# Optimization experiments

Hardware: AMD Instinct MI355X
Metric: run time of the kernel (lower is better)

Reference implementation:

```python
import jax, jax.numpy as jnp
import numpy as np

N = 21  # nodes per graph (20 laser sectors + 1 robot node)
MAX_RANGE = 10.0
_bound = np.linspace(-np.pi / 2 - 0.03, np.pi / 2, 21, dtype=np.float32)[:-1]
_angles = _bound + np.float32(np.pi / 20)
ANGLE_FEAT = jnp.asarray(np.stack([np.sin(_angles), np.cos(_angles)], 1), dtype=jnp.float32)  # [20,2]


def _build_nodes(state24):
    # state24: [B,24] -> node features [B,21,7]
    B = state24.shape[0]
    laser = state24[:, :20, None] / MAX_RANGE                       # [B,20,1]
    angle = jnp.broadcast_to(ANGLE_FEAT[None], (B, 20, 2))          # [B,20,2]
    sector = jnp.concatenate([laser, angle, jnp.zeros((B, 20, 4), state24.dtype)], -1)  # [B,20,7]
    robot = jnp.concatenate([jnp.zeros((B, 1, 3), state24.dtype), state24[:, None, 20:]], -1)  # [B,1,7]
    return jnp.concatenate([sector, robot], axis=1)                 # [B,21,7]


def _gatv2(x, Wl, Wr, att, bias, heads, dim):
    # GATv2 over a fully-connected graph with self-loops (dense all-pairs).
    # e_ij = att . leaky_relu(Wl x_j + Wr x_i); alpha = softmax_j; out_i = sum_j alpha_ij (Wl x_j)
    B = x.shape[0]
    gl = (x @ Wl).reshape(B, N, heads, dim)  # source transform [B,j,H,D]
    gr = (x @ Wr).reshape(B, N, heads, dim)  # target transform [B,i,H,D]
    s = jax.nn.leaky_relu(gl[:, None] + gr[:, :, None], negative_slope=0.2)  # [B,i,j,H,D]
    e = jnp.einsum('bijhd,hd->bijh', s, att)                                  # [B,i,j,H]
    alpha = jax.nn.softmax(e, axis=2)                                          # softmax over sources j
    out = jnp.einsum('bijh,bjhd->bihd', alpha, gl).reshape(B, N, heads * dim)
    return out + bias


def setup_inputs() -> dict:
    key = jax.random.key(0)
    ks = jax.random.split(key, 16)
    r = lambda k, shape, s: (jax.random.normal(k, shape, dtype=jnp.float32) * s)
    B = 1024
    return {
        'state24': jax.random.normal(ks[0], (B, 24), dtype=jnp.float32),
        'Wl1': r(ks[1], (7, 256), 0.3), 'Wr1': r(ks[2], (7, 256), 0.3),
        'att1': r(ks[3], (4, 64), 0.1), 'b1': r(ks[4], (256,), 0.02),
        'Wl2': r(ks[5], (256, 64), 0.06), 'Wr2': r(ks[6], (256, 64), 0.06),
        'att2': r(ks[7], (1, 64), 0.1), 'b2': r(ks[8], (64,), 0.02),
        'fc1_w': r(ks[9], (64, 256), 0.12), 'fc1_b': r(ks[10], (256,), 0.02),
        'fc2_w': r(ks[11], (256, 256), 0.06), 'fc2_b': r(ks[12], (256,), 0.02),
        'fc3_w': r(ks[13], (256, 2), 0.06), 'fc3_b': r(ks[14], (2,), 0.02),
    }


def reference(state24, Wl1, Wr1, att1, b1, Wl2, Wr2, att2, b2,
              fc1_w, fc1_b, fc2_w, fc2_b, fc3_w, fc3_b):
    x = _build_nodes(state24)                               # [B,21,7]
    h = jax.nn.elu(_gatv2(x, Wl1, Wr1, att1, b1, 4, 64))    # [B,21,256]
    h = _gatv2(h, Wl2, Wr2, att2, b2, 1, 64)                # [B,21,64]
    nfv = jnp.mean(h, axis=1)                               # global_mean_pool -> [B,64]
    h = jax.nn.relu(nfv @ fc1_w + fc1_b)
    h = jax.nn.relu(h @ fc2_w + fc2_b)
    return jnp.tanh(h @ fc3_w + fc3_b)                      # [B,2]
```

## Files before the change

kernel.cpp:

```cpp
#include <hip/hip_runtime.h>
#include <hip/hip_fp16.h>
#include <math.h>

#define PI_D 3.141592653589793

typedef _Float16 h2 __attribute__((ext_vector_type(2)));
typedef _Float16 h4 __attribute__((ext_vector_type(4)));
typedef _Float16 h8 __attribute__((ext_vector_type(8)));
typedef unsigned short us8 __attribute__((ext_vector_type(8)));
typedef __fp16 f16v2 __attribute__((ext_vector_type(2)));
typedef __fp16 f16v8 __attribute__((ext_vector_type(8)));
typedef float f32x4 __attribute__((ext_vector_type(4)));

#define STR1 264
#define STR2H 72

#define SV(v, a, b) __builtin_shufflevector(v, v, a, b)

static __device__ __forceinline__ h2 pack_h2(float a, float b) {
    return __builtin_bit_cast(h2, __builtin_amdgcn_cvt_pkrtz(a, b));
}

static __device__ __forceinline__ float fdot2(h2 a, h2 b, float c) {
    return __builtin_amdgcn_fdot2(__builtin_bit_cast(f16v2, a),
                                  __builtin_bit_cast(f16v2, b), c, false);
}

static __device__ __forceinline__ h8 habs8(h8 x) {
    us8 u = __builtin_bit_cast(us8, x);
    us8 m = {0x7fff, 0x7fff, 0x7fff, 0x7fff, 0x7fff, 0x7fff, 0x7fff, 0x7fff};
    return __builtin_bit_cast(h8, (us8)(u & m));
}

static __device__ __forceinline__ f32x4 mfma16(h8 a, h8 b, f32x4 c) {
    return __builtin_amdgcn_mfma_f32_16x16x32_f16(
        __builtin_bit_cast(f16v8, a), __builtin_bit_cast(f16v8, b), c, 0, 0, 0);
}

static __device__ __forceinline__ void wave_fence() {
    asm volatile("" ::: "memory");
#if __has_builtin(__builtin_amdgcn_wave_barrier)
    __builtin_amdgcn_wave_barrier();
#endif
    asm volatile("" ::: "memory");
}

__global__ __launch_bounds__(256) void pack_weights_kernel(
    const float* __restrict__ Wl2, const float* __restrict__ Wr2,
    const float* __restrict__ fc1_w, const float* __restrict__ fc2_w,
    h8* __restrict__ ws)
{
    int idx = blockIdx.x * 256 + threadIdx.x;
    if (idx < 4096) {
        const float* W = idx < 2048 ? Wl2 : Wr2;
        int t = idx & 2047;
        int ntile = t >> 9, rem = t & 511;
        int kchunk = rem >> 6, lane = rem & 63;
        int n = ntile * 16 + (lane & 15);
        int k0 = kchunk * 32 + (lane >> 4) * 8;
        h8 o;
        #pragma unroll
        for (int j = 0; j < 8; ++j) o[j] = (_Float16)W[(k0 + j) * 64 + n];
        ws[idx] = o;
    } else if (idx < 6144) {
        int t = idx - 4096;
        int k2 = t >> 6, c = t & 63;
        h8 o;
        #pragma unroll
        for (int q = 0; q < 4; ++q) {
            o[2 * q]     = (_Float16)fc1_w[(2 * k2) * 256 + 4 * c + q];
            o[2 * q + 1] = (_Float16)fc1_w[(2 * k2 + 1) * 256 + 4 * c + q];
        }
        ws[idx] = o;
    } else {
        int t = idx - 6144;
        int k2 = t >> 6, c = t & 63;
        h8 o;
        #pragma unroll
        for (int q = 0; q < 4; ++q) {
            o[2 * q]     = (_Float16)fc2_w[(2 * k2) * 256 + 4 * c + q];
            o[2 * q + 1] = (_Float16)fc2_w[(2 * k2 + 1) * 256 + 4 * c + q];
        }
        ws[idx] = o;
    }
}

__global__ __launch_bounds__(256, 2) void actor_fused_kernel(
    const float* __restrict__ state24,
    const float* __restrict__ Wl1, const float* __restrict__ Wr1,
    const float* __restrict__ att1, const float* __restrict__ b1,
    const float* __restrict__ att2, const float* __restrict__ b2,
    const float* __restrict__ fc1_b, const float* __restrict__ fc2_b,
    const float* __restrict__ fc3_w, const float* __restrict__ fc3_b,
    const h8* __restrict__ wsL, const h8* __restrict__ wsR,
    const h8* __restrict__ wsF1, const h8* __restrict__ wsF2,
    float* __restrict__ out, int B)
{
    const int bix = blockIdx.x;
    const int tid = threadIdx.x;
    const int smp0 = 2 * bix;
    if (smp0 >= B) return;
    const int smp1 = (smp0 + 1 < B) ? smp0 + 1 : smp0;

    __shared__ float sinL[20], cosL[20], laserL[2][20], robotL[2][4];
    __shared__ __align__(16) h2 attLh[128];
    __shared__ __align__(16) h2 att2Lh[32];
    __shared__ __align__(16) _Float16 gr1h[2][22 * STR1];
    __shared__ __align__(16) union {
        struct { _Float16 gl1h[2][22 * STR1];
                 float ePf[2][128 * 24];
                 float uv[2][168]; } p1;
        struct { _Float16 gl2h[2][21 * STR2H];
                 _Float16 gr2h[2][21 * STR2H];
                 _Float16 gl2hT[2][64 * 32];
                 float e2[2][32 * 24];
                 float u2v2[2][42];
                 float red[2][4][256];
                 _Float16 nfvh[2][64]; _Float16 hah[2][256]; _Float16 hbh[2][256]; } p2;
    } U;

    if (tid < 20) {
        double step = (PI_D + 0.03) / 20.0;
        float bound = (float)(-PI_D / 2.0 - 0.03 + (double)tid * step);
        float ang = bound + (float)(PI_D / 20.0);
        sinL[tid] = sinf(ang);
        cosL[tid] = cosf(ang);
        laserL[0][tid] = state24[smp0 * 24 + tid] * 0.1f;
        laserL[1][tid] = state24[smp1 * 24 + tid] * 0.1f;
    }
    if (tid >= 32 && tid < 40) {
        int s = (tid - 32) >> 2, q = (tid - 32) & 3;
        robotL[s][q] = state24[(s ? smp1 : smp0) * 24 + 20 + q];
    }
    if (tid < 128) {
        float2 ap = ((const float2*)att1)[tid];
        attLh[tid] = pack_h2(0.4f * ap.x, 0.4f * ap.y);
    }
    if (tid >= 128 && tid < 160) {
        float2 ap = ((const float2*)att2)[tid - 128];
        att2Lh[tid - 128] = pack_h2(0.4f * ap.x, 0.4f * ap.y);
    }
    __syncthreads();

    {
        const int h = tid >> 6;
        const int lane = tid & 63;

        {
            const int cp = lane & 31;
            const int half = lane >> 5;
            const int d2 = h * 32 + cp;
            float2 wl[7], wr[7];
            #pragma unroll
            for (int k = 0; k < 7; k++) {
                wl[k] = ((const float2*)Wl1)[k * 128 + d2];
                wr[k] = ((const float2*)Wr1)[k * 128 + d2];
            }
            if (half == 0) {
                h2 zz2 = {};
                #pragma unroll
                for (int s = 0; s < 2; ++s) {
                    ((h2*)(U.p1.gl1h[s] + 21 * STR1))[d2] = zz2;
                    ((h2*)(gr1h[s] + 21 * STR1))[d2] = zz2;
                }
            }
            const int base = half * 11;
            #pragma unroll
            for (int nn = 0; nn < 11; ++nn) {
                int node = base + nn;
                if (node < 21) {
                    #pragma unroll
                    for (int s = 0; s < 2; ++s) {
                        float a0, a1, b0, b1v;
                        if (node < 20) {
                            float l = laserL[s][node], sv = sinL[node], c = cosL[node];
                            a0 = l * wl[0].x + sv * wl[1].x + c * wl[2].x;
                            a1 = l * wl[0].y + sv * wl[1].y + c * wl[2].y;
                            b0 = l * wr[0].x + sv * wr[1].x + c * wr[2].x;
                            b1v = l * wr[0].y + sv * wr[1].y + c * wr[2].y;
                        } else {
                            float r0 = robotL[s][0], r1 = robotL[s][1], r2 = robotL[s][2], r3 = robotL[s][3];
                            a0 = r0 * wl[3].x + r1 * wl[4].x + r2 * wl[5].x + r3 * wl[6].x;
                            a1 = r0 * wl[3].y + r1 * wl[4].y + r2 * wl[5].y + r3 * wl[6].y;
                            b0 = r0 * wr[3].x + r1 * wr[4].x + r2 * wr[5].x + r3 * wr[6].x;
                            b1v = r0 * wr[3].y + r1 * wr[4].y + r2 * wr[5].y + r3 * wr[6].y;
                        }
                        ((h2*)(U.p1.gl1h[s] + node * STR1))[d2] = pack_h2(a0, a1);
                        ((h2*)(gr1h[s] + node * STR1))[d2] = pack_h2(b0, b1v);
                    }
                }
            }
        }
        wave_fence();

        {
            h2 ar[32];
            #pragma unroll
            for (int q = 0; q < 32; ++q) ar[q] = attLh[h * 32 + q];

            #pragma unroll
            for (int s = 0; s < 2; ++s) {
                for (int it = 0; it < 7; ++it) {
                    int q = it * 64 + lane;
                    if (q < 441) {
                        int i = q / 21;
                        int j = q - i * 21;
                        const h8* gA8 = (const h8*)(U.p1.gl1h[s] + j * STR1 + h * 64);
                        const h8* gB8 = (const h8*)(gr1h[s] + i * STR1 + h * 64);
                        float m0 = 0.f, m1 = 0.f;
                        #pragma unroll
                        for (int ch = 0; ch < 8; ++ch) {
                            h8 x = gA8[ch] + gB8[ch];
                            h8 ax = habs8(x);
                            m0 = fdot2(SV(ax, 0, 1), ar[ch * 4 + 0], m0);
                            m1 = fdot2(SV(ax, 2, 3), ar[ch * 4 + 1], m1);
                            m0 = fdot2(SV(ax, 4, 5), ar[ch * 4 + 2], m0);
                            m1 = fdot2(SV(ax, 6, 7), ar[ch * 4 + 3], m1);
                        }
                        U.p1.ePf[s][(h * 32 + i) * 24 + j] = m0 + m1;
                    }
                }
            }
            if (lane < 42) {
                int isV = lane >= 21;
                int idx = isV ? lane - 21 : lane;
                #pragma unroll
                for (int s = 0; s < 2; ++s) {
                    const _Float16* rowp = (isV ? (const _Float16*)gr1h[s]
                                                : (const _Float16*)U.p1.gl1h[s]) + idx * STR1 + h * 64;
                    const h8* row8 = (const h8*)rowp;
                    float l0 = 0.f, l1 = 0.f;
                    #pragma unroll
                    for (int ch = 0; ch < 8; ++ch) {
                        h8 g = row8[ch];
                        l0 = fdot2(SV(g, 0, 1), ar[ch * 4 + 0], l0);
                        l1 = fdot2(SV(g, 2, 3), ar[ch * 4 + 1], l1);
                        l0 = fdot2(SV(g, 4, 5), ar[ch * 4 + 2], l0);
                        l1 = fdot2(SV(g, 6, 7), ar[ch * 4 + 3], l1);
                    }
                    U.p1.uv[s][(isV ? 84 : 0) + h * 21 + idx] = l0 + l1;
                }
            }
        }
        wave_fence();

        if (lane < 42) {
            int s = lane >= 21;
            int i = lane - s * 21;
            int r = h * 32 + i;
            float* row = U.p1.ePf[s] + r * 24;
            const float* uu = U.p1.uv[s] + h * 21;
            float vi = 1.5f * U.p1.uv[s][84 + h * 21 + i];
            float ebuf[21];
            float m = -1e30f;
            #pragma unroll
            for (int j = 0; j < 21; j++) {
                float e = row[j] + 1.5f * uu[j] + vi;
                ebuf[j] = e;
                m = fmaxf(m, e);
            }
            float sum = 0.f;
            #pragma unroll
            for (int j = 0; j < 21; j++) { float v = __expf(ebuf[j] - m); ebuf[j] = v; sum += v; }
            float rinv = 1.f / sum;
            h8* hp8 = (h8*)(U.p1.ePf[s]) + r * 6;
            h8 o0, o1, o2;
            #pragma unroll
            for (int q = 0; q < 8; ++q) o0[q] = (_Float16)(ebuf[q] * rinv);
            #pragma unroll
            for (int q = 0; q < 8; ++q) o1[q] = (_Float16)(ebuf[8 + q] * rinv);
            #pragma unroll
            for (int q = 0; q < 5; ++q) o2[q] = (_Float16)(ebuf[16 + q] * rinv);
            o2[5] = (_Float16)0.f; o2[6] = (_Float16)0.f; o2[7] = (_Float16)0.f;
            h8 zz = {};
            hp8[0] = o0; hp8[1] = o1; hp8[2] = o2;
            hp8[3] = zz; hp8[4] = zz; hp8[5] = zz;
        }
        {
            h8 zz = {};
            for (int z = lane; z < 132; z += 64) {
                int s = z >= 66;
                int zz2 = z - s * 66;
                int rr = zz2 / 6, slot = zz2 - rr * 6;
                ((h8*)U.p1.ePf[s])[(h * 32 + 21 + rr) * 6 + slot] = zz;
            }
        }
        wave_fence();

        {
            const int mcol = lane & 15;
            const int quad = lane >> 4;
            h8 A0s[2], A1s[2];
            #pragma unroll
            for (int s = 0; s < 2; ++s) {
                const h8* Af = (const h8*)U.p1.ePf[s];
                A0s[s] = Af[(h * 32 + mcol) * 6 + quad];
                A1s[s] = Af[(h * 32 + 16 + mcol) * 6 + quad];
            }
            int rowoff[8];
            #pragma unroll
            for (int jj = 0; jj < 8; ++jj) {
                int rr = quad * 8 + jj;
                rowoff[jj] = (rr > 21 ? 21 : rr) * STR1;
            }
            const int colbase = h * 64 + mcol;
            f32x4 z4 = {0.f, 0.f, 0.f, 0.f};
            #pragma unroll
            for (int t = 0; t < 4; ++t) {
                int col = colbase + t * 16;
                float bb = b1[col];
                #pragma unroll
                for (int s = 0; s < 2; ++s) {
                    h8 bv;
                    #pragma unroll
                    for (int jj = 0; jj < 8; ++jj) bv[jj] = U.p1.gl1h[s][rowoff[jj] + col];
                    f32x4 d0 = mfma16(A0s[s], bv, z4);
                    f32x4 d1 = mfma16(A1s[s], bv, z4);
                    #pragma unroll
                    for (int r = 0; r < 4; ++r) {
                        int n0 = quad * 4 + r;
                        float v = d0[r] + bb;
                        v = v > 0.f ? v : __expf(v) - 1.f;
                        gr1h[s][n0 * STR1 + col] = (_Float16)v;
                        int n1 = 16 + quad * 4 + r;
                        if (n1 < 21) {
                            float w2 = d1[r] + bb;
                            w2 = w2 > 0.f ? w2 : __expf(w2) - 1.f;
                            gr1h[s][n1 * STR1 + col] = (_Float16)w2;
                        }
                    }
                }
            }
        }
    }
    __syncthreads();

    {
        const int lane = tid & 63;
        const int w = tid >> 6;
        const int mrow = lane & 15;
        const int quad = lane >> 4;
        int rowA1 = 16 + mrow; if (rowA1 > 21) rowA1 = 21;
        const h8* bL = wsL + w * 512 + lane;
        const h8* bR = wsR + w * 512 + lane;
        f32x4 aL0[2], aL1[2], aR0[2], aR1[2];
        #pragma unroll
        for (int s = 0; s < 2; ++s) {
            aL0[s] = (f32x4){0.f, 0.f, 0.f, 0.f}; aL1[s] = (f32x4){0.f, 0.f, 0.f, 0.f};
            aR0[s] = (f32x4){0.f, 0.f, 0.f, 0.f}; aR1[s] = (f32x4){0.f, 0.f, 0.f, 0.f};
        }
        #pragma unroll
        for (int kc = 0; kc < 8; ++kc) {
            h8 BL = bL[kc * 64];
            h8 BR = bR[kc * 64];
            #pragma unroll
            for (int s = 0; s < 2; ++s) {
                h8 A0 = *(const h8*)(gr1h[s] + mrow * STR1 + quad * 8 + kc * 32);
                h8 A1 = *(const h8*)(gr1h[s] + rowA1 * STR1 + quad * 8 + kc * 32);
                aL0[s] = mfma16(A0, BL, aL0[s]);
                aL1[s] = mfma16(A1, BL, aL1[s]);
                aR0[s] = mfma16(A0, BR, aR0[s]);
                aR1[s] = mfma16(A1, BR, aR1[s]);
            }
        }
        const int col = w * 16 + mrow;
        #pragma unroll
        for (int s = 0; s < 2; ++s) {
            #pragma unroll
            for (int r = 0; r < 4; ++r) {
                int row0 = quad * 4 + r;
                U.p2.gl2h[s][row0 * STR2H + col] = (_Float16)aL0[s][r];
                U.p2.gr2h[s][row0 * STR2H + col] = (_Float16)aR0[s][r];
                int row1 = 16 + row0;
                if (row1 < 21) {
                    U.p2.gl2h[s][row1 * STR2H + col] = (_Float16)aL1[s][r];
                    U.p2.gr2h[s][row1 * STR2H + col] = (_Float16)aR1[s][r];
                }
            }
            h2 lo0 = pack_h2(aL0[s][0], aL0[s][1]);
            h2 hi0 = pack_h2(aL0[s][2], aL0[s][3]);
            h4 p0 = __builtin_shufflevector(lo0, hi0, 0, 1, 2, 3);
            *(h4*)(U.p2.gl2hT[s] + col * 32 + quad * 4) = p0;
            h2 lo1 = pack_h2(aL1[s][0], aL1[s][1]);
            h2 hi1 = pack_h2(aL1[s][2], aL1[s][3]);
            h4 p1 = __builtin_shufflevector(lo1, hi1, 0, 1, 2, 3);
            *(h4*)(U.p2.gl2hT[s] + col * 32 + 16 + quad * 4) = p1;
        }
    }
    __syncthreads();

    {
        h2 ar2[32];
        #pragma unroll
        for (int q = 0; q < 32; ++q) ar2[q] = att2Lh[q];

        #pragma unroll
        for (int it = 0; it < 4; ++it) {
            int t = it * 256 + tid;
            if (t < 882) {
                int s = t >= 441;
                int p = t - s * 441;
                int i = p / 21;
                int j = p - i * 21;
                const h8* gA8 = (const h8*)(U.p2.gl2h[s] + j * STR2H);
                const h8* gB8 = (const h8*)(U.p2.gr2h[s] + i * STR2H);
                float m0 = 0.f, m1 = 0.f;
                #pragma unroll
                for (int ch = 0; ch < 8; ++ch) {
                    h8 x = gA8[ch] + gB8[ch];
                    h8 ax = habs8(x);
                    m0 = fdot2(SV(ax, 0, 1), ar2[ch * 4 + 0], m0);
                    m1 = fdot2(SV(ax, 2, 3), ar2[ch * 4 + 1], m1);
                    m0 = fdot2(SV(ax, 4, 5), ar2[ch * 4 + 2], m0);
                    m1 = fdot2(SV(ax, 6, 7), ar2[ch * 4 + 3], m1);
                }
                U.p2.e2[s][i * 24 + j] = m0 + m1;
            } else if (t < 966) {
                int u = t - 882;
                int s = u >= 42;
                int r = u - s * 42;
                int isV = r >= 21;
                int idx = r - isV * 21;
                const _Float16* rowp = (isV ? U.p2.gr2h[s] : U.p2.gl2h[s]) + idx * STR2H;
                const h8* row8 = (const h8*)rowp;
                float l0 = 0.f, l1 = 0.f;
                #pragma unroll
                for (int ch = 0; ch < 8; ++ch) {
                    h8 g = row8[ch];
                    l0 = fdot2(SV(g, 0, 1), ar2[ch * 4 + 0], l0);
                    l1 = fdot2(SV(g, 2, 3), ar2[ch * 4 + 1], l1);
                    l0 = fdot2(SV(g, 4, 5), ar2[ch * 4 + 2], l0);
                    l1 = fdot2(SV(g, 6, 7), ar2[ch * 4 + 3], l1);
                }
                U.p2.u2v2[s][isV * 21 + idx] = l0 + l1;
            }
        }
    }
    __syncthreads();

    if (tid < 42) {
        int s = tid >= 21;
        int i = tid - s * 21;
        float* row = U.p2.e2[s] + i * 24;
        const float* uu = U.p2.u2v2[s];
        float vi = 1.5f * U.p2.u2v2[s][21 + i];
        float ebuf[21];
        float m = -1e30f;
        #pragma unroll
        for (int j = 0; j < 21; j++) {
            float e = row[j] + 1.5f * uu[j] + vi;
            ebuf[j] = e;
            m = fmaxf(m, e);
        }
        float sum = 0.f;
        #pragma unroll
        for (int j = 0; j < 21; j++) { float v = __expf(ebuf[j] - m); ebuf[j] = v; sum += v; }
        float rinv = 1.f / sum;
        h8* hp8 = (h8*)(U.p2.e2[s]) + i * 6;
        h8 o0, o1, o2;
        #pragma unroll
        for (int q = 0; q < 8; ++q) o0[q] = (_Float16)(ebuf[q] * rinv);
        #pragma unroll
        for (int q = 0; q < 8; ++q) o1[q] = (_Float16)(ebuf[8 + q] * rinv);
        #pragma unroll
        for (int q = 0; q < 5; ++q) o2[q] = (_Float16)(ebuf[16 + q] * rinv);
        o2[5] = (_Float16)0.f; o2[6] = (_Float16)0.f; o2[7] = (_Float16)0.f;
        h8 zz = {};
        hp8[0] = o0; hp8[1] = o1; hp8[2] = o2;
        hp8[3] = zz; hp8[4] = zz; hp8[5] = zz;
    } else if (tid < 174) {
        int z = tid - 42;
        int s = z >= 66;
        int zz2 = z - s * 66;
        int rr = zz2 / 6, slot = zz2 - rr * 6;
        h8 zz = {};
        ((h8*)U.p2.e2[s])[(21 + rr) * 6 + slot] = zz;
    }
    __syncthreads();

    {
        const int lane = tid & 63;
        const int w = tid >> 6;
        const int mcol = lane & 15;
        const int quad = lane >> 4;
        const int col = w * 16 + mcol;
        float bb = b2[col];
        f32x4 z4 = {0.f, 0.f, 0.f, 0.f};
        #pragma unroll
        for (int s = 0; s < 2; ++s) {
            const h8* Af2 = (const h8*)U.p2.e2[s];
            h8 A0 = Af2[mcol * 6 + quad];
            h8 A1 = Af2[(16 + mcol) * 6 + quad];
            h8 bv = *(const h8*)(U.p2.gl2hT[s] + col * 32 + quad * 8);
            f32x4 d0 = mfma16(A0, bv, z4);
            f32x4 d1 = mfma16(A1, bv, z4);
            float sum = (d0[0] + d0[1]) + (d0[2] + d0[3])
                      + (d1[0] + d1[1]) + (d1[2] + d1[3]);
            sum += __shfl_xor(sum, 16, 64);
            sum += __shfl_xor(sum, 32, 64);
            if (quad == 0) U.p2.nfvh[s][col] = (_Float16)(sum * (1.f / 21.f) + bb);
        }
    }
    __syncthreads();

    {
        int c = tid & 63, g = tid >> 6;
        float4 acc0 = {0.f, 0.f, 0.f, 0.f}, acc1 = {0.f, 0.f, 0.f, 0.f};
        #pragma unroll
        for (int kk = 0; kk < 8; ++kk) {
            int k2 = g * 8 + kk;
            h8 w = wsF1[k2 * 64 + c];
            h2 x0 = ((const h2*)U.p2.nfvh[0])[k2];
            h2 x1 = ((const h2*)U.p2.nfvh[1])[k2];
            acc0.x = fdot2(SV(w, 0, 1), x0, acc0.x);
            acc0.y = fdot2(SV(w, 2, 3), x0, acc0.y);
            acc0.z = fdot2(SV(w, 4, 5), x0, acc0.z);
            acc0.w = fdot2(SV(w, 6, 7), x0, acc0.w);
            acc1.x = fdot2(SV(w, 0, 1), x1, acc1.x);
            acc1.y = fdot2(SV(w, 2, 3), x1, acc1.y);
            acc1.z = fdot2(SV(w, 4, 5), x1, acc1.z);
            acc1.w = fdot2(SV(w, 6, 7), x1, acc1.w);
        }
        ((float4*)U.p2.red[0][g])[c] = acc0;
        ((float4*)U.p2.red[1][g])[c] = acc1;
    }
    __syncthreads();
    {
        float bb = fc1_b[tid];
        #pragma unroll
        for (int s = 0; s < 2; ++s) {
            float v = U.p2.red[s][0][tid] + U.p2.red[s][1][tid]
                    + U.p2.red[s][2][tid] + U.p2.red[s][3][tid] + bb;
            U.p2.hah[s][tid] = (_Float16)fmaxf(v, 0.f);
        }
    }
    __syncthreads();

    {
        int c = tid & 63, g = tid >> 6;
        const h8* ha0 = (const h8*)U.p2.hah[0];
        const h8* ha1 = (const h8*)U.p2.hah[1];
        float4 acc0 = {0.f, 0.f, 0.f, 0.f}, acc1 = {0.f, 0.f, 0.f, 0.f};
#define FC2_STEP(q, p)                                                          \
        {                                                                       \
            int k2 = g * 32 + (q) * 4 + (p);                                    \
            h8 w = wsF2[k2 * 64 + c];                                           \
            h2 x0 = __builtin_shufflevector(xa0, xa0, 2 * (p), 2 * (p) + 1);    \
            h2 x1 = __builtin_shufflevector(xa1, xa1, 2 * (p), 2 * (p) + 1);    \
            acc0.x = fdot2(SV(w, 0, 1), x0, acc0.x);                            \
            acc0.y = fdot2(SV(w, 2, 3), x0, acc0.y);                            \
            acc0.z = fdot2(SV(w, 4, 5), x0, acc0.z);                            \
            acc0.w = fdot2(SV(w, 6, 7), x0, acc0.w);                            \
            acc1.x = fdot2(SV(w, 0, 1), x1, acc1.x);                            \
            acc1.y = fdot2(SV(w, 2, 3), x1, acc1.y);                            \
            acc1.z = fdot2(SV(w, 4, 5), x1, acc1.z);                            \
            acc1.w = fdot2(SV(w, 6, 7), x1, acc1.w);                            \
        }
        #pragma unroll
        for (int q = 0; q < 8; ++q) {
            h8 xa0 = ha0[g * 8 + q];
            h8 xa1 = ha1[g * 8 + q];
            FC2_STEP(q, 0)
            FC2_STEP(q, 1)
            FC2_STEP(q, 2)
            FC2_STEP(q, 3)
        }
#undef FC2_STEP
        ((float4*)U.p2.red[0][g])[c] = acc0;
        ((float4*)U.p2.red[1][g])[c] = acc1;
    }
    __syncthreads();
    {
        float bb = fc2_b[tid];
        #pragma unroll
        for (int s = 0; s < 2; ++s) {
            float v = U.p2.red[s][0][tid] + U.p2.red[s][1][tid]
                    + U.p2.red[s][2][tid] + U.p2.red[s][3][tid] + bb;
            U.p2.hbh[s][tid] = (_Float16)fmaxf(v, 0.f);
        }
    }
    __syncthreads();

    {
        int g = tid >> 6;
        int o = g & 1, s = g >> 1;
        int l = tid & 63;
        float sum = 0.f;
        #pragma unroll
        for (int m = 0; m < 4; m++) {
            int k = l + 64 * m;
            sum = fmaf((float)U.p2.hbh[s][k], fc3_w[k * 2 + o], sum);
        }
        #pragma unroll
        for (int off = 32; off >= 1; off >>= 1) sum += __shfl_down(sum, off, 64);
        if (l == 0 && smp0 + s < B) out[(smp0 + s) * 2 + o] = tanhf(sum + fc3_b[o]);
    }
}

extern "C" void kernel_launch(void* const* d_in, const int* in_sizes, int n_in,
                              void* d_out, int out_size, void* d_ws, size_t ws_size,
                              hipStream_t stream) {
    const float* state24 = (const float*)d_in[0];
    const float* Wl1 = (const float*)d_in[1];
    const float* Wr1 = (const float*)d_in[2];
    const float* att1 = (const float*)d_in[3];
    const float* b1 = (const float*)d_in[4];
    const float* Wl2 = (const float*)d_in[5];
    const float* Wr2 = (const float*)d_in[6];
    const float* att2 = (const float*)d_in[7];
    const float* b2 = (const float*)d_in[8];
    const float* fc1_w = (const float*)d_in[9];
    const float* fc1_b = (const float*)d_in[10];
    const float* fc2_w = (const float*)d_in[11];
    const float* fc2_b = (const float*)d_in[12];
    const float* fc3_w = (const float*)d_in[13];
    const float* fc3_b = (const float*)d_in[14];
    float* out = (float*)d_out;

    h8* ws = (h8*)d_ws;
    const h8* wsL = ws;
    const h8* wsR = ws + 2048;
    const h8* wsF1 = ws + 4096;
    const h8* wsF2 = ws + 6144;

    pack_weights_kernel<<<56, 256, 0, stream>>>(Wl2, Wr2, fc1_w, fc2_w, ws);

    int B = in_sizes[0] / 24;
    int nb = (B + 1) / 2;
    actor_fused_kernel<<<nb, 256, 0, stream>>>(
        state24, Wl1, Wr1, att1, b1, att2, b2,
        fc1_b, fc2_b, fc3_w, fc3_b,
        wsL, wsR, wsF1, wsF2, out, B);
}
```

Baseline: 111.7 us.

## Process four samples per block instead of two to amortize weight loads

Each block now handles four batch samples (NS=4) instead of two, so the global weight fragments used by the layer-2 MFMA, fc1 and fc2 steps are loaded once and applied to more samples. Shared-memory buffers double in size and launch bounds drop to one block per SM, while the grid shrinks to B/4 blocks. This trades occupancy and parallelism (256 blocks for B=1024) for less repeated weight traffic, and it raises register pressure from the larger per-sample accumulator arrays.

```diff
diff --git a/kernel.cpp b/kernel.cpp
--- a/kernel.cpp
+++ b/kernel.cpp
@@ -14,6 +14,7 @@
 
 #define STR1 264
 #define STR2H 72
+#define NS 4
 
 #define SV(v, a, b) __builtin_shufflevector(v, v, a, b)
 
@@ -85,7 +86,7 @@
     }
 }
 
-__global__ __launch_bounds__(256, 2) void actor_fused_kernel(
+__global__ __launch_bounds__(256, 1) void actor_fused_kernel(
     const float* __restrict__ state24,
     const float* __restrict__ Wl1, const float* __restrict__ Wr1,
     const float* __restrict__ att1, const float* __restrict__ b1,
@@ -98,25 +99,24 @@
 {
     const int bix = blockIdx.x;
     const int tid = threadIdx.x;
-    const int smp0 = 2 * bix;
-    if (smp0 >= B) return;
-    const int smp1 = (smp0 + 1 < B) ? smp0 + 1 : smp0;
-
-    __shared__ float sinL[20], cosL[20], laserL[2][20], robotL[2][4];
+    const int smpb = NS * bix;
+    if (smpb >= B) return;
+
+    __shared__ float sinL[20], cosL[20], laserL[NS][20], robotL[NS][4];
     __shared__ __align__(16) h2 attLh[128];
     __shared__ __align__(16) h2 att2Lh[32];
-    __shared__ __align__(16) _Float16 gr1h[2][22 * STR1];
+    __shared__ __align__(16) _Float16 gr1h[NS][22 * STR1];
     __shared__ __align__(16) union {
-        struct { _Float16 gl1h[2][22 * STR1];
-                 float ePf[2][128 * 24];
-                 float uv[2][168]; } p1;
-        struct { _Float16 gl2h[2][21 * STR2H];
-                 _Float16 gr2h[2][21 * STR2H];
-                 _Float16 gl2hT[2][64 * 32];
-                 float e2[2][32 * 24];
-                 float u2v2[2][42];
-                 float red[2][4][256];
-                 _Float16 nfvh[2][64]; _Float16 hah[2][256]; _Float16 hbh[2][256]; } p2;
+        struct { _Float16 gl1h[NS][22 * STR1];
+                 float ePf[NS][128 * 24];
+                 float uv[NS][168]; } p1;
+        struct { _Float16 gl2h[NS][21 * STR2H];
+                 _Float16 gr2h[NS][21 * STR2H];
+                 _Float16 gl2hT[NS][64 * 32];
+                 float e2[NS][32 * 24];
+                 float u2v2[NS][42];
+                 float red[NS][4][256];
+                 _Float16 nfvh[NS][64]; _Float16 hah[NS][256]; _Float16 hbh[NS][256]; } p2;
     } U;
 
     if (tid < 20) {
@@ -125,12 +125,16 @@
         float ang = bound + (float)(PI_D / 20.0);
         sinL[tid] = sinf(ang);
         cosL[tid] = cosf(ang);
-        laserL[0][tid] = state24[smp0 * 24 + tid] * 0.1f;
-        laserL[1][tid] = state24[smp1 * 24 + tid] * 0.1f;
-    }
-    if (tid >= 32 && tid < 40) {
+        #pragma unroll
+        for (int s = 0; s < NS; ++s) {
+            int sm = smpb + s; if (sm >= B) sm = B - 1;
+            laserL[s][tid] = state24[sm * 24 + tid] * 0.1f;
+        }
+    }
+    if (tid >= 32 && tid < 32 + 4 * NS) {
         int s = (tid - 32) >> 2, q = (tid - 32) & 3;
-        robotL[s][q] = state24[(s ? smp1 : smp0) * 24 + 20 + q];
+        int sm = smpb + s; if (sm >= B) sm = B - 1;
+        robotL[s][q] = state24[sm * 24 + 20 + q];
     }
     if (tid < 128) {
         float2 ap = ((const float2*)att1)[tid];
@@ -159,7 +163,7 @@
             if (half == 0) {
                 h2 zz2 = {};
                 #pragma unroll
-                for (int s = 0; s < 2; ++s) {
+                for (int s = 0; s < NS; ++s) {
                     ((h2*)(U.p1.gl1h[s] + 21 * STR1))[d2] = zz2;
                     ((h2*)(gr1h[s] + 21 * STR1))[d2] = zz2;
                 }
@@ -170,7 +174,7 @@
                 int node = base + nn;
                 if (node < 21) {
                     #pragma unroll
-                    for (int s = 0; s < 2; ++s) {
+                    for (int s = 0; s < NS; ++s) {
                         float a0, a1, b0, b1v;
                         if (node < 20) {
                             float l = laserL[s][node], sv = sinL[node], c = cosL[node];
@@ -199,7 +203,7 @@
             for (int q = 0; q < 32; ++q) ar[q] = attLh[h * 32 + q];
 
             #pragma unroll
-            for (int s = 0; s < 2; ++s) {
+            for (int s = 0; s < NS; ++s) {
                 for (int it = 0; it < 7; ++it) {
                     int q = it * 64 + lane;
                     if (q < 441) {
@@ -225,7 +229,7 @@
                 int isV = lane >= 21;
                 int idx = isV ? lane - 21 : lane;
                 #pragma unroll
-                for (int s = 0; s < 2; ++s) {
+                for (int s = 0; s < NS; ++s) {
                     const _Float16* rowp = (isV ? (const _Float16*)gr1h[s]
                                                 : (const _Float16*)U.p1.gl1h[s]) + idx * STR1 + h * 64;
                     const h8* row8 = (const h8*)rowp;
@@ -244,9 +248,9 @@
         }
         wave_fence();
 
-        if (lane < 42) {
-            int s = lane >= 21;
-            int i = lane - s * 21;
+        for (int z = lane; z < 84; z += 64) {
+            int s = z / 21;
+            int i = z - s * 21;
             int r = h * 32 + i;
             float* row = U.p1.ePf[s] + r * 24;
             const float* uu = U.p1.uv[s] + h * 21;
@@ -278,8 +282,8 @@
         }
         {
             h8 zz = {};
-            for (int z = lane; z < 132; z += 64) {
-                int s = z >= 66;
+            for (int z = lane; z < 66 * NS; z += 64) {
+                int s = z / 66;
                 int zz2 = z - s * 66;
                 int rr = zz2 / 6, slot = zz2 - rr * 6;
                 ((h8*)U.p1.ePf[s])[(h * 32 + 21 + rr) * 6 + slot] = zz;
@@ -290,9 +294,9 @@
         {
             const int mcol = lane & 15;
             const int quad = lane >> 4;
-            h8 A0s[2], A1s[2];
-            #pragma unroll
-            for (int s = 0; s < 2; ++s) {
+            h8 A0s[NS], A1s[NS];
+            #pragma unroll
+            for (int s = 0; s < NS; ++s) {
                 const h8* Af = (const h8*)U.p1.ePf[s];
                 A0s[s] = Af[(h * 32 + mcol) * 6 + quad];
                 A1s[s] = Af[(h * 32 + 16 + mcol) * 6 + quad];
@@ -310,7 +314,7 @@
                 int col = colbase + t * 16;
                 float bb = b1[col];
                 #pragma unroll
-                for (int s = 0; s < 2; ++s) {
+                for (int s = 0; s < NS; ++s) {
                     h8 bv;
                     #pragma unroll
                     for (int jj = 0; jj < 8; ++jj) bv[jj] = U.p1.gl1h[s][rowoff[jj] + col];
@@ -343,9 +347,9 @@
         int rowA1 = 16 + mrow; if (rowA1 > 21) rowA1 = 21;
         const h8* bL = wsL + w * 512 + lane;
         const h8* bR = wsR + w * 512 + lane;
-        f32x4 aL0[2], aL1[2], aR0[2], aR1[2];
-        #pragma unroll
-        for (int s = 0; s < 2; ++s) {
+        f32x4 aL0[NS], aL1[NS], aR0[NS], aR1[NS];
+        #pragma unroll
+        for (int s = 0; s < NS; ++s) {
             aL0[s] = (f32x4){0.f, 0.f, 0.f, 0.f}; aL1[s] = (f32x4){0.f, 0.f, 0.f, 0.f};
             aR0[s] = (f32x4){0.f, 0.f, 0.f, 0.f}; aR1[s] = (f32x4){0.f, 0.f, 0.f, 0.f};
         }
@@ -354,7 +358,7 @@
             h8 BL = bL[kc * 64];
             h8 BR = bR[kc * 64];
             #pragma unroll
-            for (int s = 0; s < 2; ++s) {
+            for (int s = 0; s < NS; ++s) {
                 h8 A0 = *(const h8*)(gr1h[s] + mrow * STR1 + quad * 8 + kc * 32);
                 h8 A1 = *(const h8*)(gr1h[s] + rowA1 * STR1 + quad * 8 + kc * 32);
                 aL0[s] = mfma16(A0, BL, aL0[s]);
@@ -365,7 +369,7 @@
         }
         const int col = w * 16 + mrow;
         #pragma unroll
-        for (int s = 0; s < 2; ++s) {
+        for (int s = 0; s < NS; ++s) {
             #pragma unroll
             for (int r = 0; r < 4; ++r) {
                 int row0 = quad * 4 + r;
@@ -395,10 +399,10 @@
         for (int q = 0; q < 32; ++q) ar2[q] = att2Lh[q];
 
         #pragma unroll
-        for (int it = 0; it < 4; ++it) {
+        for (int it = 0; it < 8; ++it) {
             int t = it * 256 + tid;
-            if (t < 882) {
-                int s = t >= 441;
+            if (t < 441 * NS) {
+                int s = t / 441;
                 int p = t - s * 441;
                 int i = p / 21;
                 int j = p - i * 21;
@@ -415,9 +419,9 @@
                     m1 = fdot2(SV(ax, 6, 7), ar2[ch * 4 + 3], m1);
                 }
                 U.p2.e2[s][i * 24 + j] = m0 + m1;
-            } else if (t < 966) {
-                int u = t - 882;
-                int s = u >= 42;
+            } else if (t < 441 * NS + 42 * NS) {
+                int u = t - 441 * NS;
+                int s = u / 42;
                 int r = u - s * 42;
                 int isV = r >= 21;
                 int idx = r - isV * 21;
@@ -438,8 +442,8 @@
     }
     __syncthreads();
 
-    if (tid < 42) {
-        int s = tid >= 21;
+    if (tid < 21 * NS) {
+        int s = tid / 21;
         int i = tid - s * 21;
         float* row = U.p2.e2[s] + i * 24;
         const float* uu = U.p2.u2v2[s];
@@ -468,13 +472,14 @@
         h8 zz = {};
         hp8[0] = o0; hp8[1] = o1; hp8[2] = o2;
         hp8[3] = zz; hp8[4] = zz; hp8[5] = zz;
-    } else if (tid < 174) {
-        int z = tid - 42;
-        int s = z >= 66;
-        int zz2 = z - s * 66;
-        int rr = zz2 / 6, slot = zz2 - rr * 6;
+    } else {
         h8 zz = {};
-        ((h8*)U.p2.e2[s])[(21 + rr) * 6 + slot] = zz;
+        for (int z = tid - 21 * NS; z < 66 * NS; z += 256 - 21 * NS) {
+            int s = z / 66;
+            int zz2 = z - s * 66;
+            int rr = zz2 / 6, slot = zz2 - rr * 6;
+            ((h8*)U.p2.e2[s])[(21 + rr) * 6 + slot] = zz;
+        }
     }
     __syncthreads();
 
@@ -487,7 +492,7 @@
         float bb = b2[col];
         f32x4 z4 = {0.f, 0.f, 0.f, 0.f};
         #pragma unroll
-        for (int s = 0; s < 2; ++s) {
+        for (int s = 0; s < NS; ++s) {
             const h8* Af2 = (const h8*)U.p2.e2[s];
             h8 A0 = Af2[mcol * 6 + quad];
             h8 A1 = Af2[(16 + mcol) * 6 + quad];
@@ -505,30 +510,30 @@
 
     {
         int c = tid & 63, g = tid >> 6;
-        float4 acc0 = {0.f, 0.f, 0.f, 0.f}, acc1 = {0.f, 0.f, 0.f, 0.f};
+        float4 acc[NS];
+        #pragma unroll
+        for (int s = 0; s < NS; ++s) acc[s] = (float4){0.f, 0.f, 0.f, 0.f};
         #pragma unroll
         for (int kk = 0; kk < 8; ++kk) {
             int k2 = g * 8 + kk;
             h8 w = wsF1[k2 * 64 + c];
-            h2 x0 = ((const h2*)U.p2.nfvh[0])[k2];
-            h2 x1 = ((const h2*)U.p2.nfvh[1])[k2];
-            acc0.x = fdot2(SV(w, 0, 1), x0, acc0.x);
-            acc0.y = fdot2(SV(w, 2, 3), x0, acc0.y);
-            acc0.z = fdot2(SV(w, 4, 5), x0, acc0.z);
-            acc0.w = fdot2(SV(w, 6, 7), x0, acc0.w);
-            acc1.x = fdot2(SV(w, 0, 1), x1, acc1.x);
-            acc1.y = fdot2(SV(w, 2, 3), x1, acc1.y);
-            acc1.z = fdot2(SV(w, 4, 5), x1, acc1.z);
-            acc1.w = fdot2(SV(w, 6, 7), x1, acc1.w);
-        }
-        ((float4*)U.p2.red[0][g])[c] = acc0;
-        ((float4*)U.p2.red[1][g])[c] = acc1;
+            #pragma unroll
+            for (int s = 0; s < NS; ++s) {
+                h2 x = ((const h2*)U.p2.nfvh[s])[k2];
+                acc[s].x = fdot2(SV(w, 0, 1), x, acc[s].x);
+                acc[s].y = fdot2(SV(w, 2, 3), x, acc[s].y);
+                acc[s].z = fdot2(SV(w, 4, 5), x, acc[s].z);
+                acc[s].w = fdot2(SV(w, 6, 7), x, acc[s].w);
+            }
+        }
+        #pragma unroll
+        for (int s = 0; s < NS; ++s) ((float4*)U.p2.red[s][g])[c] = acc[s];
     }
     __syncthreads();
     {
         float bb = fc1_b[tid];
         #pragma unroll
-        for (int s = 0; s < 2; ++s) {
+        for (int s = 0; s < NS; ++s) {
             float v = U.p2.red[s][0][tid] + U.p2.red[s][1][tid]
                     + U.p2.red[s][2][tid] + U.p2.red[s][3][tid] + bb;
             U.p2.hah[s][tid] = (_Float16)fmaxf(v, 0.f);
@@ -538,42 +543,41 @@
 
     {
         int c = tid & 63, g = tid >> 6;
-        const h8* ha0 = (const h8*)U.p2.hah[0];
-        const h8* ha1 = (const h8*)U.p2.hah[1];
-        float4 acc0 = {0.f, 0.f, 0.f, 0.f}, acc1 = {0.f, 0.f, 0.f, 0.f};
+        float4 acc[NS];
+        #pragma unroll
+        for (int s = 0; s < NS; ++s) acc[s] = (float4){0.f, 0.f, 0.f, 0.f};
 #define FC2_STEP(q, p)                                                          \
         {                                                                       \
             int k2 = g * 32 + (q) * 4 + (p);                                    \
             h8 w = wsF2[k2 * 64 + c];                                           \
-            h2 x0 = __builtin_shufflevector(xa0, xa0, 2 * (p), 2 * (p) + 1);    \
-            h2 x1 = __builtin_shufflevector(xa1, xa1, 2 * (p), 2 * (p) + 1);    \
-            acc0.x = fdot2(SV(w, 0, 1), x0, acc0.x);                            \
-            acc0.y = fdot2(SV(w, 2, 3), x0, acc0.y);                            \
-            acc0.z = fdot2(SV(w, 4, 5), x0, acc0.z);                            \
-            acc0.w = fdot2(SV(w, 6, 7), x0, acc0.w);                            \
-            acc1.x = fdot2(SV(w, 0, 1), x1, acc1.x);                            \
-            acc1.y = fdot2(SV(w, 2, 3), x1, acc1.y);                            \
-            acc1.z = fdot2(SV(w, 4, 5), x1, acc1.z);                            \
-            acc1.w = fdot2(SV(w, 6, 7), x1, acc1.w);                            \
+            _Pragma("unroll")                                                   \
+            for (int s = 0; s < NS; ++s) {                                      \
+                h2 x = __builtin_shufflevector(xa[s], xa[s], 2 * (p), 2 * (p) + 1); \
+                acc[s].x = fdot2(SV(w, 0, 1), x, acc[s].x);                     \
+                acc[s].y = fdot2(SV(w, 2, 3), x, acc[s].y);                     \
+                acc[s].z = fdot2(SV(w, 4, 5), x, acc[s].z);                     \
+                acc[s].w = fdot2(SV(w, 6, 7), x, acc[s].w);                     \
+            }                                                                   \
         }
         #pragma unroll
         for (int q = 0; q < 8; ++q) {
-            h8 xa0 = ha0[g * 8 + q];
-            h8 xa1 = ha1[g * 8 + q];
+            h8 xa[NS];
+            #pragma unroll
+            for (int s = 0; s < NS; ++s) xa[s] = ((const h8*)U.p2.hah[s])[g * 8 + q];
             FC2_STEP(q, 0)
             FC2_STEP(q, 1)
             FC2_STEP(q, 2)
             FC2_STEP(q, 3)
         }
 #undef FC2_STEP
-        ((float4*)U.p2.red[0][g])[c] = acc0;
-        ((float4*)U.p2.red[1][g])[c] = acc1;
+        #pragma unroll
+        for (int s = 0; s < NS; ++s) ((float4*)U.p2.red[s][g])[c] = acc[s];
     }
     __syncthreads();
     {
         float bb = fc2_b[tid];
         #pragma unroll
-        for (int s = 0; s < 2; ++s) {
+        for (int s = 0; s < NS; ++s) {
             float v = U.p2.red[s][0][tid] + U.p2.red[s][1][tid]
                     + U.p2.red[s][2][tid] + U.p2.red[s][3][tid] + bb;
             U.p2.hbh[s][tid] = (_Float16)fmaxf(v, 0.f);
@@ -582,18 +586,30 @@
     __syncthreads();
 
     {
-        int g = tid >> 6;
-        int o = g & 1, s = g >> 1;
+        int s = tid >> 6;
         int l = tid & 63;
-        float sum = 0.f;
-        #pragma unroll
-        for (int m = 0; m < 4; m++) {
-            int k = l + 64 * m;
-            sum = fmaf((float)U.p2.hbh[s][k], fc3_w[k * 2 + o], sum);
-        }
-        #pragma unroll
-        for (int off = 32; off >= 1; off >>= 1) sum += __shfl_down(sum, off, 64);
-        if (l == 0 && smp0 + s < B) out[(smp0 + s) * 2 + o] = tanhf(sum + fc3_b[o]);
+        float w0 = fc3_w[l * 2 + 0],       w1 = fc3_w[l * 2 + 1];
+        float w2 = fc3_w[(l + 64) * 2],    w3 = fc3_w[(l + 64) * 2 + 1];
+        float w4 = fc3_w[(l + 128) * 2],   w5 = fc3_w[(l + 128) * 2 + 1];
+        float w6 = fc3_w[(l + 192) * 2],   w7 = fc3_w[(l + 192) * 2 + 1];
+        float h0 = (float)U.p2.hbh[s][l];
+        float h1 = (float)U.p2.hbh[s][l + 64];
+        float h2v = (float)U.p2.hbh[s][l + 128];
+        float h3 = (float)U.p2.hbh[s][l + 192];
+        float s0 = h0 * w0 + h1 * w2 + h2v * w4 + h3 * w6;
+        float s1 = h0 * w1 + h1 * w3 + h2v * w5 + h3 * w7;
+        #pragma unroll
+        for (int off = 32; off >= 1; off >>= 1) {
+            s0 += __shfl_down(s0, off, 64);
+            s1 += __shfl_down(s1, off, 64);
+        }
+        if (l == 0) {
+            int sm = smpb + s;
+            if (sm < B) {
+                out[sm * 2 + 0] = tanhf(s0 + fc3_b[0]);
+                out[sm * 2 + 1] = tanhf(s1 + fc3_b[1]);
+            }
+        }
     }
 }
 
@@ -626,7 +642,7 @@
     pack_weights_kernel<<<56, 256, 0, stream>>>(Wl2, Wr2, fc1_w, fc2_w, ws);
 
     int B = in_sizes[0] / 24;
-    int nb = (B + 1) / 2;
+    int nb = (B + NS - 1) / NS;
     actor_fused_kernel<<<nb, 256, 0, stream>>>(
         state24, Wl1, Wr1, att1, b1, att2, b2,
         fc1_b, fc2_b, fc3_w, fc3_b,
```

After: 122.8 us. 9.9% more time.
